# Optimization experiments

Measured on AMD Instinct MI355X. Metric: run time of the kernel, lower is better.

The kernel has to match this reference:

```python
import jax, jax.numpy as jnp
import numpy as np

EMBED_DIM = 1024
NUM_HEADS = 16
HEAD_DIM = EMBED_DIM // NUM_HEADS
NEG_INF = -1e9


def setup_inputs() -> dict:
    key = jax.random.key(0)
    k1, k2, k3, k4, k5 = jax.random.split(key, 5)
    # ragged batch: 8 segments, alternating lengths 1024 / 512 -> 6144 tokens
    lengths = np.array([1024, 512, 1024, 512, 1024, 512, 1024, 512], dtype=np.int32)
    cu_seqlens = np.concatenate([[0], np.cumsum(lengths)]).astype(np.int32)
    total = int(cu_seqlens[-1])  # 6144
    scale = 0.02
    return {
        "hidden_states": jax.random.normal(k1, (total, EMBED_DIM), dtype=jnp.float32),
        "proj_weight": jax.random.normal(k2, (3 * EMBED_DIM, EMBED_DIM), dtype=jnp.float32) * scale,
        "proj_bias": jax.random.normal(k3, (3 * EMBED_DIM,), dtype=jnp.float32) * scale,
        "out_weight": jax.random.normal(k4, (EMBED_DIM, EMBED_DIM), dtype=jnp.float32) * scale,
        "out_bias": jax.random.normal(k5, (EMBED_DIM,), dtype=jnp.float32) * scale,
        "cu_seqlens": jnp.asarray(cu_seqlens),
        "max_len": 1024,
    }


def reference(hidden_states, proj_weight, proj_bias, out_weight, out_bias, cu_seqlens, max_len):
    T = hidden_states.shape[0]
    B = cu_seqlens.shape[0] - 1
    H, Dh = NUM_HEADS, HEAD_DIM
    softmax_scale = 1.0 / jnp.sqrt(jnp.float32(Dh))

    # fused QKV projection: [T, 3E] -> [T, H, 3, Dh]
    qkv = hidden_states @ proj_weight.T + proj_bias
    qkv = qkv.reshape(T, H, 3, Dh)
    q, k, v = qkv[:, :, 0], qkv[:, :, 1], qkv[:, :, 2]  # each [T, H, Dh]

    # unpack ragged tokens into padded [B, S, H, Dh]
    lengths = cu_seqlens[1:] - cu_seqlens[:-1]            # [B]
    pos = jnp.arange(max_len)                              # [S]
    valid = pos[None, :] < lengths[:, None]                # [B, S]
    idx = jnp.where(valid, cu_seqlens[:-1, None] + pos[None, :], 0)  # [B, S]
    qp, kp, vp = q[idx], k[idx], v[idx]                    # [B, S, H, Dh]

    # per-segment attention (non-causal encoder self-attn)
    scores = jnp.einsum("bqhd,bkhd->bhqk", qp, kp) * softmax_scale  # [B,H,S,S]
    scores = jnp.where(valid[:, None, None, :], scores, NEG_INF)
    probs = jax.nn.softmax(scores, axis=-1)
    ctx = jnp.einsum("bhqk,bkhd->bqhd", probs, vp)         # [B, S, H, Dh]

    # pack back to ragged [T, E]; invalid slots scattered out-of-bounds (dropped)
    scatter_idx = jnp.where(valid, idx, T).reshape(-1)     # [B*S]
    ctx_flat = ctx.reshape(B * max_len, H * Dh)
    context = jnp.zeros((T, H * Dh), dtype=ctx_flat.dtype).at[scatter_idx].set(
        ctx_flat, mode="drop")

    return context @ out_weight.T + out_bias
```

## Files before the change

kernel.cpp:

```cpp
#include <hip/hip_runtime.h>
#include <math.h>

#define EMBED 1024
#define NHEAD 16
#define HDIM 64
#define QKV_LD 3072
#define SM_SCALE_LOG2 0.18033688f

typedef _Float16 f16x8 __attribute__((ext_vector_type(8)));
typedef float f32x4 __attribute__((ext_vector_type(4)));
typedef unsigned short ushort8v __attribute__((ext_vector_type(8)));
typedef unsigned short ushort4v __attribute__((ext_vector_type(4)));

__device__ __forceinline__ void gload16(const void* g, void* l) {
    __builtin_amdgcn_global_load_lds(
        (const __attribute__((address_space(1))) unsigned int*)g,
        (__attribute__((address_space(3))) unsigned int*)l, 16, 0, 0);
}

__device__ __forceinline__ int xcd_swz(int bid, int nwg) {
    int cpx = nwg >> 3;
    return (bid & 7) * cpx + (bid >> 3);
}

__device__ __forceinline__ int swz(int row, int col) {
    return row * 72 + (col ^ (((row >> 3) & 7) << 3));
}

__global__ __launch_bounds__(256) void cvt_f32_f16(
    const float* __restrict__ x, _Float16* __restrict__ y, int n4)
{
    int i = blockIdx.x * 256 + threadIdx.x;
    if (i >= n4) return;
    float4 v = reinterpret_cast<const float4*>(x)[i];
    unsigned short h0 = __builtin_bit_cast(unsigned short, (_Float16)v.x);
    unsigned short h1 = __builtin_bit_cast(unsigned short, (_Float16)v.y);
    unsigned short h2 = __builtin_bit_cast(unsigned short, (_Float16)v.z);
    unsigned short h3 = __builtin_bit_cast(unsigned short, (_Float16)v.w);
    reinterpret_cast<ushort4*>(y)[i] = make_ushort4(h0, h1, h2, h3);
}

template <bool F16_OUT>
__global__ __launch_bounds__(256) void gemm_m97(
    const _Float16* __restrict__ A, const _Float16* __restrict__ B,
    const float* __restrict__ bias, float* __restrict__ Cf,
    _Float16* __restrict__ Ch, int M, int N, int K, int gx)
{
    __shared__ __align__(16) unsigned short sA[128 * 64];
    __shared__ __align__(16) unsigned short sB[128 * 64];

    const int nwg = gridDim.x;
    const int wgid = xcd_swz(blockIdx.x, nwg);
    const int row0 = (wgid / gx) * 128;
    const int col0 = (wgid % gx) * 128;

    const int tid = threadIdx.x;
    const int lane = tid & 63;
    const int w = tid >> 6;
    const int wr = w >> 1;
    const int wc = w & 1;
    const int c = lane & 15;
    const int g = lane >> 4;

    const unsigned short* Au = (const unsigned short*)A;
    const unsigned short* Bu = (const unsigned short*)B;

    f32x4 acc[4][4];
    #pragma unroll
    for (int m = 0; m < 4; m++)
        #pragma unroll
        for (int n = 0; n < 4; n++)
            acc[m][n] = (f32x4){0.f, 0.f, 0.f, 0.f};

    size_t aoff[4], boff[4];
    int ldst[4];
    #pragma unroll
    for (int i = 0; i < 4; i++) {
        int chunk = (i * 4 + w) * 64 + lane;
        int row = chunk >> 3;
        int scol = ((chunk & 7) ^ (row & 7)) * 8;
        aoff[i] = (size_t)min(row0 + row, M - 1) * K + scol;
        boff[i] = (size_t)min(col0 + row, N - 1) * K + scol;
        ldst[i] = chunk * 8;
    }

    for (int k0 = 0; k0 < K; k0 += 64) {
        __syncthreads();
        #pragma unroll
        for (int i = 0; i < 4; i++) {
            gload16(Au + aoff[i] + k0, &sA[ldst[i]]);
            gload16(Bu + boff[i] + k0, &sB[ldst[i]]);
        }
        __syncthreads();

        #pragma unroll
        for (int ks = 0; ks < 2; ks++) {
            f16x8 af[4], bf[4];
            #pragma unroll
            for (int m = 0; m < 4; m++) {
                int row = wr * 64 + m * 16 + c;
                int cc = (ks * 4 + g) ^ (row & 7);
                af[m] = __builtin_bit_cast(f16x8, *reinterpret_cast<const ushort8v*>(
                            &sA[row * 64 + cc * 8]));
            }
            #pragma unroll
            for (int n = 0; n < 4; n++) {
                int row = wc * 64 + n * 16 + c;
                int cc = (ks * 4 + g) ^ (row & 7);
                bf[n] = __builtin_bit_cast(f16x8, *reinterpret_cast<const ushort8v*>(
                            &sB[row * 64 + cc * 8]));
            }
            #pragma unroll
            for (int m = 0; m < 4; m++)
                #pragma unroll
                for (int n = 0; n < 4; n++)
                    acc[m][n] = __builtin_amdgcn_mfma_f32_16x16x32_f16(af[m], bf[n], acc[m][n], 0, 0, 0);
        }
    }

    #pragma unroll
    for (int m = 0; m < 4; m++) {
        #pragma unroll
        for (int n = 0; n < 4; n++) {
            int cc = col0 + wc * 64 + n * 16 + c;
            if (cc >= N) continue;
            float bv = bias[cc];
            #pragma unroll
            for (int j = 0; j < 4; j++) {
                int r = row0 + wr * 64 + m * 16 + g * 4 + j;
                if (r >= M) continue;
                float v = acc[m][n][j] + bv;
                if constexpr (F16_OUT) {
                    Ch[(size_t)r * N + cc] = (_Float16)v;
                } else {
                    Cf[(size_t)r * N + cc] = v;
                }
            }
        }
    }
}

__global__ __launch_bounds__(256) void attn_mfma(
    const _Float16* __restrict__ qkv, const int* __restrict__ cu,
    _Float16* __restrict__ ctx, int B, int maxTiles)
{
    __shared__ __align__(16) unsigned short sK[64 * 72];
    __shared__ __align__(16) unsigned short sV[64 * 72];

    const int nwg = gridDim.x;
    const int wgid = xcd_swz(blockIdx.x, nwg);
    const int h = wgid / maxTiles;
    const int tile = wgid % maxTiles;

    int b = -1, q0 = 0, accum = 0;
    for (int i = 0; i < B; i++) {
        int len = cu[i + 1] - cu[i];
        int nt = (len + 63) >> 6;
        if (tile < accum + nt) { b = i; q0 = (tile - accum) << 6; break; }
        accum += nt;
    }
    if (b < 0) return;
    const int s0 = cu[b];
    const int L = cu[b + 1] - s0;
    if (q0 >= L) return;

    const int tid = threadIdx.x;
    const int lane = tid & 63;
    const int w = tid >> 6;
    const int g = lane >> 4;
    const int c = lane & 15;
    const size_t qcol = (size_t)h * 192;
    const unsigned short* qkvu = (const unsigned short*)qkv;

    f16x8 q[2];
    {
        int qrow = min(q0 + w * 16 + c, L - 1);
        size_t off = (size_t)(s0 + qrow) * QKV_LD + qcol + g * 8;
        q[0] = *reinterpret_cast<const f16x8*>(&qkv[off]);
        q[1] = *reinterpret_cast<const f16x8*>(&qkv[off + 32]);
    }

    f32x4 o[4];
    #pragma unroll
    for (int n = 0; n < 4; n++) o[n] = (f32x4){0.f, 0.f, 0.f, 0.f};
    float m_r = -INFINITY;
    float l_r = 0.f;

    for (int kc = 0; kc < L; kc += 64) {
        __syncthreads();
        #pragma unroll
        for (int it = 0; it < 2; it++) {
            int idx = it * 256 + tid;
            int r = idx >> 3;
            int d0 = (idx & 7) * 8;
            int gr = min(kc + r, L - 1);
            size_t off = (size_t)(s0 + gr) * QKV_LD + qcol + 64 + d0;
            *reinterpret_cast<uint4*>(&sK[swz(r, d0)]) =
                *reinterpret_cast<const uint4*>(&qkvu[off]);
            ushort8v vv = *reinterpret_cast<const ushort8v*>(&qkvu[off + 64]);
            #pragma unroll
            for (int j = 0; j < 8; j++)
                sV[swz(d0 + j, r)] = vv[j];
        }
        __syncthreads();

        __builtin_amdgcn_s_setprio(1);
        f32x4 sacc[4];
        #pragma unroll
        for (int f = 0; f < 4; f++) sacc[f] = (f32x4){0.f, 0.f, 0.f, 0.f};
        #pragma unroll
        for (int f = 0; f < 4; f++) {
            #pragma unroll
            for (int ks = 0; ks < 2; ks++) {
                f16x8 kf = __builtin_bit_cast(f16x8, *reinterpret_cast<const ushort8v*>(
                               &sK[swz(f * 16 + c, ks * 32 + g * 8)]));
                sacc[f] = __builtin_amdgcn_mfma_f32_16x16x32_f16(kf, q[ks], sacc[f], 0, 0, 0);
            }
        }
        __builtin_amdgcn_s_setprio(0);

        float mx = -INFINITY;
        if (kc + 64 <= L) {
            #pragma unroll
            for (int f = 0; f < 4; f++) {
                #pragma unroll
                for (int j = 0; j < 4; j++) {
                    float v = sacc[f][j] * SM_SCALE_LOG2;
                    sacc[f][j] = v;
                    mx = fmaxf(mx, v);
                }
            }
        } else {
            #pragma unroll
            for (int f = 0; f < 4; f++) {
                #pragma unroll
                for (int j = 0; j < 4; j++) {
                    float v = sacc[f][j] * SM_SCALE_LOG2;
                    if (kc + f * 16 + g * 4 + j >= L) v = -1.0e9f;
                    sacc[f][j] = v;
                    mx = fmaxf(mx, v);
                }
            }
        }
        mx = fmaxf(mx, __shfl_xor(mx, 16));
        mx = fmaxf(mx, __shfl_xor(mx, 32));

        const bool nskip = !__all(mx - m_r <= 8.0f);
        const float mn = nskip ? fmaxf(m_r, mx) : m_r;

        unsigned int paw[4][2];
        float rs = 0.f;
        #pragma unroll
        for (int f = 0; f < 4; f++) {
            float p0 = exp2f(sacc[f][0] - mn);
            float p1 = exp2f(sacc[f][1] - mn);
            float p2 = exp2f(sacc[f][2] - mn);
            float p3 = exp2f(sacc[f][3] - mn);
            rs += (p0 + p1) + (p2 + p3);
            unsigned int h0 = __builtin_bit_cast(unsigned short, (_Float16)p0);
            unsigned int h1 = __builtin_bit_cast(unsigned short, (_Float16)p1);
            unsigned int h2 = __builtin_bit_cast(unsigned short, (_Float16)p2);
            unsigned int h3 = __builtin_bit_cast(unsigned short, (_Float16)p3);
            paw[f][0] = h0 | (h1 << 16);
            paw[f][1] = h2 | (h3 << 16);
        }
        rs += __shfl_xor(rs, 16);
        rs += __shfl_xor(rs, 32);

        if (nskip) {
            float fs = exp2f(m_r - mn);
            l_r = l_r * fs + rs;
            m_r = mn;
            #pragma unroll
            for (int j = 0; j < 4; j++) {
                float fq = __shfl(fs, (lane & 48) | (g * 4 + j));
                #pragma unroll
                for (int n = 0; n < 4; n++)
                    o[n][j] *= fq;
            }
        } else {
            l_r += rs;
        }

        __builtin_amdgcn_s_setprio(1);
        #pragma unroll
        for (int ks = 0; ks < 2; ks++) {
            uint4 pw;
            pw.x = paw[2 * ks][0];
            pw.y = paw[2 * ks][1];
            pw.z = paw[2 * ks + 1][0];
            pw.w = paw[2 * ks + 1][1];
            f16x8 pa = __builtin_bit_cast(f16x8, pw);
            #pragma unroll
            for (int n = 0; n < 4; n++) {
                uint2 lo = *reinterpret_cast<const uint2*>(
                               &sV[swz(n * 16 + c, ks * 32 + g * 4)]);
                uint2 hi = *reinterpret_cast<const uint2*>(
                               &sV[swz(n * 16 + c, ks * 32 + 16 + g * 4)]);
                uint4 vw;
                vw.x = lo.x; vw.y = lo.y; vw.z = hi.x; vw.w = hi.y;
                f16x8 vf = __builtin_bit_cast(f16x8, vw);
                o[n] = __builtin_amdgcn_mfma_f32_16x16x32_f16(pa, vf, o[n], 0, 0, 0);
            }
        }
        __builtin_amdgcn_s_setprio(0);
    }

    float linv[4];
    {
        float il = 1.0f / l_r;
        #pragma unroll
        for (int j = 0; j < 4; j++)
            linv[j] = __shfl(il, (lane & 48) | (g * 4 + j));
    }
    #pragma unroll
    for (int n = 0; n < 4; n++) {
        #pragma unroll
        for (int j = 0; j < 4; j++) {
            int r = q0 + w * 16 + g * 4 + j;
            if (r >= L) continue;
            ctx[(size_t)(s0 + r) * EMBED + h * HDIM + n * 16 + c] =
                (_Float16)(o[n][j] * linv[j]);
        }
    }
}

extern "C" void kernel_launch(void* const* d_in, const int* in_sizes, int n_in,
                              void* d_out, int out_size, void* d_ws, size_t ws_size,
                              hipStream_t stream) {
    const float* hs = (const float*)d_in[0];
    const float* pw = (const float*)d_in[1];
    const float* pb = (const float*)d_in[2];
    const float* ow = (const float*)d_in[3];
    const float* ob = (const float*)d_in[4];
    const int*   cu = (const int*)d_in[5];

    const int T = in_sizes[0] / EMBED;
    const int B = in_sizes[5] - 1;

    char* p = (char*)d_ws;
    size_t hsF_b  = (size_t)T * EMBED * sizeof(_Float16);
    size_t pwF_b  = (size_t)3 * EMBED * EMBED * sizeof(_Float16);
    size_t owF_b  = (size_t)EMBED * EMBED * sizeof(_Float16);
    size_t qkvF_b = (size_t)T * QKV_LD * sizeof(_Float16);
    size_t ctxF_b = hsF_b;

    _Float16* hsF  = (_Float16*)p;  p += hsF_b;
    _Float16* pwF  = (_Float16*)p;  p += pwF_b;
    _Float16* owF  = (_Float16*)p;  p += owF_b;
    _Float16* qkvF = (_Float16*)p;  p += qkvF_b;
    _Float16* ctxF = (_Float16*)p;  p += ctxF_b;

    float* out = (float*)d_out;
    dim3 blk(256);

    {
        int n4 = T * EMBED / 4;
        cvt_f32_f16<<<(n4 + 255) / 256, blk, 0, stream>>>(hs, hsF, n4);
        n4 = 3 * EMBED * EMBED / 4;
        cvt_f32_f16<<<(n4 + 255) / 256, blk, 0, stream>>>(pw, pwF, n4);
        n4 = EMBED * EMBED / 4;
        cvt_f32_f16<<<(n4 + 255) / 256, blk, 0, stream>>>(ow, owF, n4);
    }

    {
        int gx = (3 * EMBED) / 128;
        int nwg = gx * ((T + 127) / 128);
        gemm_m97<true><<<nwg, blk, 0, stream>>>(hsF, pwF, pb,
                                                (float*)nullptr, qkvF,
                                                T, 3 * EMBED, EMBED, gx);
    }

    {
        int maxTiles = T / 64 + B;
        int nwg = NHEAD * maxTiles;
        attn_mfma<<<nwg, blk, 0, stream>>>(qkvF, cu, ctxF, B, maxTiles);
    }

    {
        int gx = EMBED / 128;
        int nwg = gx * ((T + 127) / 128);
        gemm_m97<false><<<nwg, blk, 0, stream>>>(ctxF, owF, ob,
                                                 out, (_Float16*)nullptr,
                                                 T, EMBED, EMBED, gx);
    }
}
```

Measured before the change: 180.2 us.

## Use 256x256-tile 8-wave pipelined GEMM for QKV projection

Replaces the 128x128 QKV projection GEMM with a new 256x256-tile kernel using 512 threads, 128KB of dynamic LDS double buffering, and a hand-scheduled phase loop. That loop interleaves async global-to-LDS loads with MFMA groups, using explicit barriers, waitcnt and setprio. The goal is more data reuse per tile and better overlap of memory with compute. The trade-offs are fewer workgroups (12x24=288), which risks under-filling the CUs, plus a heavy register footprint and a fragile manual schedule.

```diff
diff --git a/kernel.cpp b/kernel.cpp
--- a/kernel.cpp
+++ b/kernel.cpp
@@ -138,6 +138,164 @@
             }
         }
     }
+}
+
+template <bool F16_OUT>
+__global__ __launch_bounds__(512, 2) void gemm_256(
+    const _Float16* __restrict__ A, const _Float16* __restrict__ B,
+    const float* __restrict__ bias, float* __restrict__ Cf,
+    _Float16* __restrict__ Ch, int M, int N, int K, int gx)
+{
+    extern __shared__ __align__(16) unsigned short lds[];
+    unsigned short* sA = lds;
+    unsigned short* sB = lds + 32768;
+
+    const int nwg = gridDim.x;
+    const int wgid = xcd_swz(blockIdx.x, nwg);
+    const int row0 = (wgid / gx) * 256;
+    const int col0 = (wgid % gx) * 256;
+
+    const int tid = threadIdx.x;
+    const int lane = tid & 63;
+    const int w = tid >> 6;
+    const int wm = w >> 2;
+    const int wn = w & 3;
+    const int c = lane & 15;
+    const int g = lane >> 4;
+
+    const unsigned short* Au = (const unsigned short*)A;
+    const unsigned short* Bu = (const unsigned short*)B;
+
+    const int rr = tid >> 3;
+    const int sc = tid & 7;
+    const int lc = sc ^ (rr & 7);
+
+    const int ca0 = (0 + g) ^ (c & 7);
+    const int ca1 = (4 + g) ^ (c & 7);
+
+    const int NT = K >> 6;
+    const int NITER = NT >> 1;
+
+    f32x4 acc[8][4];
+    #pragma unroll
+    for (int m = 0; m < 8; m++)
+        #pragma unroll
+        for (int n = 0; n < 4; n++)
+            acc[m][n] = (f32x4){0.f, 0.f, 0.f, 0.f};
+
+    f16x8 af[2][2];
+    f16x8 bf[4][2];
+
+#define STG_A(BUF, KT, U) do { \
+    int kt_ = (KT) < NT ? (KT) : NT - 1; \
+    gload16(Au + (size_t)min(row0 + (U) * 64 + rr, M - 1) * K + kt_ * 64 + lc * 8, \
+            &sA[(BUF) * 16384 + ((U) * 64 + rr) * 64 + sc * 8]); \
+    gload16(Au + (size_t)min(row0 + (U) * 64 + 128 + rr, M - 1) * K + kt_ * 64 + lc * 8, \
+            &sA[(BUF) * 16384 + ((U) * 64 + 128 + rr) * 64 + sc * 8]); \
+} while (0)
+
+#define STG_B(BUF, KT, U) do { \
+    int kt_ = (KT) < NT ? (KT) : NT - 1; \
+    gload16(Bu + (size_t)min(col0 + (U) * 64 + rr, N - 1) * K + kt_ * 64 + lc * 8, \
+            &sB[(BUF) * 16384 + ((U) * 64 + rr) * 64 + sc * 8]); \
+    gload16(Bu + (size_t)min(col0 + (U) * 64 + 128 + rr, N - 1) * K + kt_ * 64 + lc * 8, \
+            &sB[(BUF) * 16384 + ((U) * 64 + 128 + rr) * 64 + sc * 8]); \
+} while (0)
+
+#define RD_A(BUF, MQ) do { \
+    _Pragma("unroll") \
+    for (int m_ = 0; m_ < 2; m_++) { \
+        af[m_][0] = __builtin_bit_cast(f16x8, *reinterpret_cast<const ushort8v*>( \
+            &sA[(BUF) * 16384 + (wm * 128 + (MQ) * 32 + m_ * 16 + c) * 64 + ca0 * 8])); \
+        af[m_][1] = __builtin_bit_cast(f16x8, *reinterpret_cast<const ushort8v*>( \
+            &sA[(BUF) * 16384 + (wm * 128 + (MQ) * 32 + m_ * 16 + c) * 64 + ca1 * 8])); \
+    } \
+} while (0)
+
+#define RD_B(BUF) do { \
+    _Pragma("unroll") \
+    for (int n_ = 0; n_ < 4; n_++) { \
+        bf[n_][0] = __builtin_bit_cast(f16x8, *reinterpret_cast<const ushort8v*>( \
+            &sB[(BUF) * 16384 + (wn * 64 + n_ * 16 + c) * 64 + ca0 * 8])); \
+        bf[n_][1] = __builtin_bit_cast(f16x8, *reinterpret_cast<const ushort8v*>( \
+            &sB[(BUF) * 16384 + (wn * 64 + n_ * 16 + c) * 64 + ca1 * 8])); \
+    } \
+} while (0)
+
+#define DO_MFMA(MQ) do { \
+    __builtin_amdgcn_s_setprio(1); \
+    _Pragma("unroll") \
+    for (int ks_ = 0; ks_ < 2; ks_++) \
+        _Pragma("unroll") \
+        for (int m_ = 0; m_ < 2; m_++) \
+            _Pragma("unroll") \
+            for (int n_ = 0; n_ < 4; n_++) \
+                acc[(MQ) * 2 + m_][n_] = __builtin_amdgcn_mfma_f32_16x16x32_f16( \
+                    af[m_][ks_], bf[n_][ks_], acc[(MQ) * 2 + m_][n_], 0, 0, 0); \
+    __builtin_amdgcn_s_setprio(0); \
+} while (0)
+
+#define PH_HEADBAR() do { __builtin_amdgcn_s_barrier(); __builtin_amdgcn_sched_barrier(0); \
+    asm volatile("s_waitcnt lgkmcnt(0)" ::: "memory"); __builtin_amdgcn_sched_barrier(0); } while (0)
+#define PH_TAILBAR() do { __builtin_amdgcn_s_barrier(); __builtin_amdgcn_sched_barrier(0); } while (0)
+#define VM6() do { asm volatile("s_waitcnt vmcnt(6)" ::: "memory"); \
+    __builtin_amdgcn_sched_barrier(0); } while (0)
+
+    STG_B(0, 0, 0); STG_B(0, 0, 1); STG_A(0, 0, 0); STG_A(0, 0, 1);
+    STG_B(1, 1, 0); STG_B(1, 1, 1); STG_A(1, 1, 0);
+    VM6();
+    PH_TAILBAR();
+
+    #pragma unroll 1
+    for (int i = 0; i < NITER; ++i) {
+        const int t1 = 2 * i + 1, t2 = 2 * i + 2, t3 = 2 * i + 3;
+        RD_B(0); RD_A(0, 0); STG_A(1, t1, 1);
+        PH_HEADBAR(); DO_MFMA(0); PH_TAILBAR();
+        RD_A(0, 1); STG_B(0, t2, 0);
+        PH_HEADBAR(); DO_MFMA(1); PH_TAILBAR();
+        RD_A(0, 2); STG_B(0, t2, 1);
+        PH_HEADBAR(); DO_MFMA(2); PH_TAILBAR();
+        RD_A(0, 3); STG_A(0, t2, 0);
+        PH_HEADBAR(); DO_MFMA(3); VM6(); PH_TAILBAR();
+        RD_B(1); RD_A(1, 0); STG_A(0, t2, 1);
+        PH_HEADBAR(); DO_MFMA(0); PH_TAILBAR();
+        RD_A(1, 1); STG_B(1, t3, 0);
+        PH_HEADBAR(); DO_MFMA(1); PH_TAILBAR();
+        RD_A(1, 2); STG_B(1, t3, 1);
+        PH_HEADBAR(); DO_MFMA(2); PH_TAILBAR();
+        RD_A(1, 3); STG_A(1, t3, 0);
+        PH_HEADBAR(); DO_MFMA(3); VM6(); PH_TAILBAR();
+    }
+
+    #pragma unroll
+    for (int mf = 0; mf < 8; mf++) {
+        #pragma unroll
+        for (int n = 0; n < 4; n++) {
+            int cc2 = col0 + wn * 64 + n * 16 + c;
+            if (cc2 >= N) continue;
+            float bv = bias[cc2];
+            #pragma unroll
+            for (int j = 0; j < 4; j++) {
+                int r = row0 + wm * 128 + mf * 16 + g * 4 + j;
+                if (r >= M) continue;
+                float v = acc[mf][n][j] + bv;
+                if constexpr (F16_OUT) {
+                    Ch[(size_t)r * N + cc2] = (_Float16)v;
+                } else {
+                    Cf[(size_t)r * N + cc2] = v;
+                }
+            }
+        }
+    }
+
+#undef STG_A
+#undef STG_B
+#undef RD_A
+#undef RD_B
+#undef DO_MFMA
+#undef PH_HEADBAR
+#undef PH_TAILBAR
+#undef VM6
 }
 
 __global__ __launch_bounds__(256) void attn_mfma(
@@ -354,6 +512,13 @@
     float* out = (float*)d_out;
     dim3 blk(256);
 
+    static bool attrSet = false;
+    if (!attrSet) {
+        hipFuncSetAttribute(reinterpret_cast<const void*>(&gemm_256<true>),
+                            hipFuncAttributeMaxDynamicSharedMemorySize, 131072);
+        attrSet = true;
+    }
+
     {
         int n4 = T * EMBED / 4;
         cvt_f32_f16<<<(n4 + 255) / 256, blk, 0, stream>>>(hs, hsF, n4);
@@ -364,11 +529,11 @@
     }
 
     {
-        int gx = (3 * EMBED) / 128;
-        int nwg = gx * ((T + 127) / 128);
-        gemm_m97<true><<<nwg, blk, 0, stream>>>(hsF, pwF, pb,
-                                                (float*)nullptr, qkvF,
-                                                T, 3 * EMBED, EMBED, gx);
+        int gx = (3 * EMBED) / 256;
+        int nwg = gx * ((T + 255) / 256);
+        gemm_256<true><<<nwg, dim3(512), 131072, stream>>>(hsF, pwF, pb,
+                                                           (float*)nullptr, qkvF,
+                                                           T, 3 * EMBED, EMBED, gx);
     }
 
     {
```

Measured after the change: 194.5 us. +7.9%, slower.
